# Optimization experiments

Measured on AMD Instinct MI355X. Metric: run time of the kernel, lower is better.

The kernel has to match this reference:

```python
import jax, jax.numpy as jnp
import numpy as np

L, HID, NH, NKV, HD, INTER = 16, 960, 15, 5, 64, 2560
VOCAB, NV, NT, PRE, SD = 49152, 192, 48, 241, 32
THETA, EPS, B = 100000.0, 1e-5, 16
GROUPS = NH // NKV


def setup_inputs() -> dict:
    key = jax.random.key(0)
    ks = jax.random.split(key, 20)
    s = 0.02
    rn = lambda k, shp: jax.random.normal(k, shp, jnp.float32) * s
    return {
        'vision_features': jax.random.normal(ks[0], (B, NV, HID), jnp.float32),
        'lang_token_ids': jax.random.randint(ks[1], (B, NT), 0, VOCAB),
        'lang_mask': jnp.ones((B, NT), dtype=bool),
        'state': jax.random.normal(ks[2], (B, SD), jnp.float32),
        'embed': rn(ks[3], (VOCAB, HID)),
        'state_w': rn(ks[4], (SD, HID)),
        'state_b': jnp.zeros((HID,), jnp.float32),
        'Wq': rn(ks[5], (L, HID, NH * HD)),
        'Wk': rn(ks[6], (L, HID, NKV * HD)),
        'Wv': rn(ks[7], (L, HID, NKV * HD)),
        'Wo': rn(ks[8], (L, NH * HD, HID)),
        'Wg': rn(ks[9], (L, HID, INTER)),
        'Wu': rn(ks[10], (L, HID, INTER)),
        'Wd': rn(ks[11], (L, INTER, HID)),
        'ln1': jnp.ones((L, HID), jnp.float32),
        'ln2': jnp.ones((L, HID), jnp.float32),
    }


def _rms(x, w):
    var = jnp.mean(jnp.square(x), axis=-1, keepdims=True)
    return x * jax.lax.rsqrt(var + EPS) * w


def _rotate_half(x):
    h = x.shape[-1] // 2
    return jnp.concatenate([-x[..., h:], x[..., :h]], axis=-1)


def _rope_tables(position_ids):
    # position_ids: [B, S] -> cos/sin: [B, S, HD]
    inv_freq = 1.0 / (THETA ** (jnp.arange(0, HD, 2, dtype=jnp.float32) / HD))
    freqs = position_ids.astype(jnp.float32)[..., None] * inv_freq  # [B,S,HD/2]
    emb = jnp.concatenate([freqs, freqs], axis=-1)
    return jnp.cos(emb), jnp.sin(emb)


def _apply_rope(x, cos, sin):
    # x: [B,S,H,D]; cos/sin: [B,S,D]
    return x * cos[:, :, None, :] + _rotate_half(x) * sin[:, :, None, :]


def _attention(q, k, v, mask2d):
    # q: [B,S,NH,HD]; k,v: [B,S,NKV,HD]; mask2d: [B,S,S] bool (query i, key j)
    kx = jnp.repeat(k, GROUPS, axis=2)  # GQA expand -> [B,S,NH,HD]
    vx = jnp.repeat(v, GROUPS, axis=2)
    scores = jnp.einsum('bihd,bjhd->bhij', q, kx) * (HD ** -0.5)
    big_neg = jnp.finfo(jnp.float32).min
    scores = jnp.where(mask2d[:, None, :, :], scores, big_neg)
    probs = jax.nn.softmax(scores, axis=-1)
    out = jnp.einsum('bhij,bjhd->bihd', probs, vx)
    return out.reshape(q.shape[0], q.shape[1], NH * HD)


def reference(vision_features, lang_token_ids, lang_mask, state,
              embed, state_w, state_b, Wq, Wk, Wv, Wo, Wg, Wu, Wd, ln1, ln2):
    lang_emb = embed[lang_token_ids] * jnp.sqrt(jnp.float32(HID))  # [B,NT,HID]
    state_emb = (state @ state_w + state_b)[:, None, :]            # [B,1,HID]
    x = jnp.concatenate([vision_features, lang_emb, state_emb], axis=1)  # [B,PRE,HID]

    pad = jnp.concatenate([jnp.ones((B, NV), bool), lang_mask.astype(bool),
                           jnp.ones((B, 1), bool)], axis=1)  # [B,PRE]
    position_ids = jnp.clip(jnp.cumsum(pad.astype(jnp.int32), axis=1) - 1, 0, None)
    cos, sin = _rope_tables(position_ids)

    att_marks = jnp.zeros((PRE,), jnp.int32).at[NV + NT:].set(1)
    cum = jnp.cumsum(att_marks)
    att2d = cum[None, :] >= cum[:, None]  # [S_q, S_kv]: key cum <= query cum
    pad2d = pad[:, :, None] & pad[:, None, :]
    mask2d = att2d[None, :, :] & pad2d  # [B,S,S]

    def layer(x, w):
        h = _rms(x, w['ln1'])
        S = h.shape[1]
        q = (h @ w['Wq']).reshape(B, S, NH, HD)
        k = (h @ w['Wk']).reshape(B, S, NKV, HD)
        v = (h @ w['Wv']).reshape(B, S, NKV, HD)
        q = _apply_rope(q, cos, sin)
        k = _apply_rope(k, cos, sin)
        a = _attention(q, k, v, mask2d)
        x = x + a @ w['Wo']
        h2 = _rms(x, w['ln2'])
        m = (jax.nn.silu(h2 @ w['Wg']) * (h2 @ w['Wu'])) @ w['Wd']
        return x + m, (k, v)

    weights = {'Wq': Wq, 'Wk': Wk, 'Wv': Wv, 'Wo': Wo,
               'Wg': Wg, 'Wu': Wu, 'Wd': Wd, 'ln1': ln1, 'ln2': ln2}
    _, (keys, values) = jax.lax.scan(layer, x, weights)
    # keys/values: [L, B, PRE, NKV, HD]
    return keys, values
```

## Files before the change

### kernel.cpp

```cpp
#include <hip/hip_runtime.h>
#include <hip/hip_bf16.h>

namespace {

typedef __bf16 bf16_t;
typedef __bf16 bf16x8 __attribute__((ext_vector_type(8)));
typedef __bf16 bf16x4 __attribute__((ext_vector_type(4)));
typedef float f32x4 __attribute__((ext_vector_type(4)));

constexpr int kL     = 16;
constexpr int kHid   = 960;
constexpr int kNH    = 15;
constexpr int kNKV   = 5;
constexpr int kHD    = 64;
constexpr int kInter = 2560;
constexpr int kNV    = 192;
constexpr int kNT    = 48;
constexpr int kPre   = 241;
constexpr int kSD    = 32;
constexpr int kB     = 16;
constexpr int kTok   = kB * kPre;
constexpr int kTokP  = 3968;
constexpr int kQKV   = 1600;
constexpr float kEps = 1e-5f;
constexpr float kSqrtHid = 30.98386677f;

constexpr size_t kWoOff     = (size_t)1664 * 960;
constexpr size_t kWgOff     = kWoOff + (size_t)1024 * 960;
constexpr size_t kWuOff     = kWgOff + (size_t)2560 * 960;
constexpr size_t kWdOff     = kWuOff + (size_t)2560 * 960;
constexpr size_t kWPerLayer = kWdOff + (size_t)1024 * 2560;

__device__ __forceinline__ void gload16(const bf16_t* g, bf16_t* l) {
  __builtin_amdgcn_global_load_lds((const __attribute__((address_space(1))) void*)g,
                                   (__attribute__((address_space(3))) void*)l, 16, 0, 0);
}

__device__ __forceinline__ void xcd_tile(int& bx, int& by) {
  int nbx = gridDim.x;
  int nwg = nbx * gridDim.y;
  int orig = blockIdx.y * nbx + blockIdx.x;
  int q = nwg >> 3, r = nwg & 7;
  int xcd = orig & 7, pos = orig >> 3;
  int swz = (xcd < r) ? (xcd * (q + 1) + pos) : (r * (q + 1) + (xcd - r) * q + pos);
  bx = swz % nbx;
  by = swz / nbx;
}

__global__ void build_x_kernel(const float* __restrict__ vision,
                               const int*   __restrict__ tokens,
                               const float* __restrict__ state,
                               const float* __restrict__ embed,
                               const float* __restrict__ sw,
                               const float* __restrict__ sb,
                               float* __restrict__ x, bf16_t* __restrict__ xb) {
  int idx = blockIdx.x * blockDim.x + threadIdx.x;
  if (idx >= kTok * kHid) return;
  int t = idx / kHid, c = idx - t * kHid;
  int b = t / kPre, s = t - b * kPre;
  float v;
  if (s < kNV) {
    v = vision[((size_t)b * kNV + s) * kHid + c];
  } else if (s < kNV + kNT) {
    int tok = tokens[b * kNT + (s - kNV)];
    v = embed[(size_t)tok * kHid + c] * kSqrtHid;
  } else {
    float acc = sb[c];
#pragma unroll
    for (int i = 0; i < kSD; ++i) acc += state[b * kSD + i] * sw[i * kHid + c];
    v = acc;
  }
  x[idx] = v;
  xb[idx] = (bf16_t)v;
}

__global__ __launch_bounds__(256)
void rowssq_kernel(const float* __restrict__ x, float* __restrict__ ssq) {
  int t = blockIdx.x;
  int tid = threadIdx.x;
  const float* xr = x + (size_t)t * kHid;
  float4 v = make_float4(0.f, 0.f, 0.f, 0.f);
  if (tid < 240) v = ((const float4*)xr)[tid];
  float ss = v.x * v.x + v.y * v.y + v.z * v.z + v.w * v.w;
#pragma unroll
  for (int off = 32; off; off >>= 1) ss += __shfl_xor(ss, off);
  __shared__ float part[4];
  if ((tid & 63) == 0) part[tid >> 6] = ss;
  __syncthreads();
  if (tid == 0) ssq[t] = part[0] + part[1] + part[2] + part[3];
}

__global__ void rope_table_kernel(float* __restrict__ cosT, float* __restrict__ sinT) {
  int idx = blockIdx.x * blockDim.x + threadIdx.x;
  if (idx >= kPre * 32) return;
  int s = idx >> 5, fi = idx & 31;
  float inv = __expf(-(2.0f * (float)fi / (float)kHD) * __logf(100000.0f));
  float fr = (float)s * inv;
  cosT[idx] = cosf(fr);
  sinT[idx] = sinf(fr);
}

__device__ void transpose_tile(const float* __restrict__ src, bf16_t* __restrict__ dst,
                               const float* __restrict__ lnw, int K, int N, int tile) {
  __shared__ float ts[64][65];
  int ntn = N >> 6;
  int tk = tile / ntn, tn = tile - tk * ntn;
  int t = threadIdx.x;
  int r = t >> 2, c0 = (t & 3) << 4;
  const float* sp = src + (size_t)((tk << 6) + r) * N + (tn << 6) + c0;
  float4 a = ((const float4*)sp)[0];
  float4 b = ((const float4*)sp)[1];
  float4 c = ((const float4*)sp)[2];
  float4 d = ((const float4*)sp)[3];
  ts[r][c0 + 0] = a.x;  ts[r][c0 + 1] = a.y;  ts[r][c0 + 2] = a.z;  ts[r][c0 + 3] = a.w;
  ts[r][c0 + 4] = b.x;  ts[r][c0 + 5] = b.y;  ts[r][c0 + 6] = b.z;  ts[r][c0 + 7] = b.w;
  ts[r][c0 + 8] = c.x;  ts[r][c0 + 9] = c.y;  ts[r][c0 +10] = c.z;  ts[r][c0 +11] = c.w;
  ts[r][c0 +12] = d.x;  ts[r][c0 +13] = d.y;  ts[r][c0 +14] = d.z;  ts[r][c0 +15] = d.w;
  __syncthreads();
  float wv[16];
#pragma unroll
  for (int i = 0; i < 16; ++i) wv[i] = lnw ? lnw[(tk << 6) + c0 + i] : 1.f;
  bf16_t* dp = dst + (size_t)((tn << 6) + r) * K + (tk << 6) + c0;
  bf16x8 o0, o1;
#pragma unroll
  for (int i = 0; i < 8; ++i) o0[i] = (bf16_t)(ts[c0 + i][r] * wv[i]);
#pragma unroll
  for (int i = 0; i < 8; ++i) o1[i] = (bf16_t)(ts[c0 + 8 + i][r] * wv[8 + i]);
  *(bf16x8*)dp = o0;
  *(bf16x8*)(dp + 8) = o1;
}

__global__ __launch_bounds__(256)
void wconv_kernel(const float* __restrict__ Wq, const float* __restrict__ Wk,
                  const float* __restrict__ Wv, const float* __restrict__ Wo,
                  const float* __restrict__ Wg, const float* __restrict__ Wu,
                  const float* __restrict__ Wd, const float* __restrict__ ln1,
                  const float* __restrict__ ln2, bf16_t* __restrict__ wall) {
  int bid = blockIdx.x;
  int l = bid / 2400, t = bid - l * 2400;
  bf16_t* wl = wall + (size_t)l * kWPerLayer;
  const float* w1 = ln1 + (size_t)l * kHid;
  const float* w2 = ln2 + (size_t)l * kHid;
  if      (t < 225)  transpose_tile(Wq + (size_t)l * 921600, wl, w1, 960, 960, t);
  else if (t < 300)  transpose_tile(Wk + (size_t)l * 307200, wl + (size_t)960 * 960, w1, 960, 320, t - 225);
  else if (t < 375)  transpose_tile(Wv + (size_t)l * 307200, wl + (size_t)1280 * 960, w1, 960, 320, t - 300);
  else if (t < 600)  transpose_tile(Wo + (size_t)l * 921600, wl + kWoOff, nullptr, 960, 960, t - 375);
  else if (t < 1200) transpose_tile(Wg + (size_t)l * 2457600, wl + kWgOff, w2, 960, 2560, t - 600);
  else if (t < 1800) transpose_tile(Wu + (size_t)l * 2457600, wl + kWuOff, w2, 960, 2560, t - 1200);
  else               transpose_tile(Wd + (size_t)l * 2457600, wl + kWdOff, nullptr, 2560, 960, t - 1800);
}


__global__ __launch_bounds__(256, 4)
void gemm_qkv_kernel(const bf16_t* __restrict__ A, const float* __restrict__ ssq,
                     const bf16_t* __restrict__ Bt,
                     bf16_t* __restrict__ qkv, float* __restrict__ outk,
                     float* __restrict__ outv,
                     const float* __restrict__ cosT, const float* __restrict__ sinT) {
  constexpr int K = kHid;
  constexpr int NT = K / 32;
  __shared__ alignas(16) bf16_t As[2][4096];
  __shared__ alignas(16) bf16_t Bs[2][2048];
  int tid = threadIdx.x;
  int bx, by;
  xcd_tile(bx, by);
  int m0 = by * 128, n0 = bx * 64;
  int lane = tid & 63, wid = tid >> 6;
  int wr = wid * 32;
  int r0 = tid >> 2, c0 = (tid & 3) * 8;
  int lr = lane & 15, lg = lane >> 4;

  const bf16_t* a0 = A + (size_t)(m0 + r0) * K + c0;
  const bf16_t* a1 = a0 + (size_t)64 * K;
  const bf16_t* b0 = Bt + (size_t)(n0 + r0) * K + c0;

  f32x4 acc[2][4];
#pragma unroll
  for (int m = 0; m < 2; ++m)
#pragma unroll
    for (int n = 0; n < 4; ++n) acc[m][n] = (f32x4){0.f, 0.f, 0.f, 0.f};

  int arow0 = (wr + lr) * 32 + lg * 8;
  int brow0 = lr * 32 + lg * 8;

  gload16(a0, &As[0][tid * 8]);
  gload16(a1, &As[0][2048 + tid * 8]);
  gload16(b0, &Bs[0][tid * 8]);
  __syncthreads();

  int cur = 0;
  for (int t = 0; t < NT; ++t) {
    if (t + 1 < NT) {
      int k1 = (t + 1) * 32;
      gload16(a0 + k1, &As[cur ^ 1][tid * 8]);
      gload16(a1 + k1, &As[cur ^ 1][2048 + tid * 8]);
      gload16(b0 + k1, &Bs[cur ^ 1][tid * 8]);
    }
    bf16x8 af[2], bfr[4];
#pragma unroll
    for (int m = 0; m < 2; ++m) af[m] = *(const bf16x8*)&As[cur][arow0 + m * 16 * 32];
#pragma unroll
    for (int n = 0; n < 4; ++n) bfr[n] = *(const bf16x8*)&Bs[cur][brow0 + n * 16 * 32];
#pragma unroll
    for (int m = 0; m < 2; ++m)
#pragma unroll
      for (int n = 0; n < 4; ++n)
        acc[m][n] = __builtin_amdgcn_mfma_f32_16x16x32_bf16(af[m], bfr[n], acc[m][n], 0, 0, 0);
    __syncthreads();
    cur ^= 1;
  }

  int cbase = n0;
  int cr4 = lg * 4;
  float srow[2][4];
#pragma unroll
  for (int m = 0; m < 2; ++m)
#pragma unroll
    for (int r = 0; r < 4; ++r)
      srow[m][r] = rsqrtf(ssq[m0 + wr + m * 16 + cr4 + r] * (1.f / 960.f) + kEps);

  if (cbase < 1280) {
    bool isQ = cbase < 960;
    float scale = isQ ? 0.125f : 1.0f;
#pragma unroll
    for (int m = 0; m < 2; ++m) {
      int row = m0 + wr + m * 16 + cr4;
#pragma unroll
      for (int r = 0; r < 4; ++r) {
        int rr = row + r;
        if (rr >= kTok) continue;
        int s = rr % kPre;
        bf16_t* qrow = qkv + (size_t)rr * kQKV + cbase;
        float* krow = outk + (size_t)rr * 320 + (cbase - 960);
#pragma unroll
        for (int n = 0; n < 2; ++n) {
          int d = n * 16 + lr;
          float c = cosT[s * 32 + d], sn = sinT[s * 32 + d];
          float lo = acc[m][n][r] * srow[m][r];
          float hi = acc[m][n + 2][r] * srow[m][r];
          float y0 = lo * c - hi * sn;
          float y1 = hi * c + lo * sn;
          qrow[d]      = (bf16_t)(y0 * scale);
          qrow[d + 32] = (bf16_t)(y1 * scale);
          if (!isQ) { krow[d] = y0; krow[d + 32] = y1; }
        }
      }
    }
  } else {
#pragma unroll
    for (int m = 0; m < 2; ++m) {
      int row = m0 + wr + m * 16 + cr4;
#pragma unroll
      for (int r = 0; r < 4; ++r) {
        int rr = row + r;
        if (rr >= kTok) continue;
        bf16_t* qrow = qkv + (size_t)rr * kQKV + cbase;
        float* vrow = outv + (size_t)rr * 320 + (cbase - 1280);
#pragma unroll
        for (int n = 0; n < 4; ++n) {
          int d = n * 16 + lr;
          float v = acc[m][n][r] * srow[m][r];
          qrow[d] = (bf16_t)v;
          vrow[d] = v;
        }
      }
    }
  }
}

__global__ __launch_bounds__(256, 4)
void gemm_res_kernel(const bf16_t* __restrict__ A, const bf16_t* __restrict__ Bt,
                     const float* __restrict__ src, float* __restrict__ C,
                     bf16_t* __restrict__ xb, float* __restrict__ ssq_out,
                     int M, int N, int K) {
  __shared__ alignas(16) bf16_t As[2][4096];
  __shared__ alignas(16) bf16_t Bs[2][2048];
  int tid = threadIdx.x;
  int bx, by;
  xcd_tile(bx, by);
  int m0 = by * 128, n0 = bx * 64;
  int lane = tid & 63, wid = tid >> 6;
  int wr = wid * 32;
  int r0 = tid >> 2, c0 = (tid & 3) * 8;
  int lr = lane & 15, lg = lane >> 4;

  const bf16_t* a0 = A + (size_t)(m0 + r0) * K + c0;
  const bf16_t* a1 = a0 + (size_t)64 * K;
  const bf16_t* b0 = Bt + (size_t)(n0 + r0) * K + c0;

  f32x4 acc[2][4];
#pragma unroll
  for (int m = 0; m < 2; ++m)
#pragma unroll
    for (int n = 0; n < 4; ++n) acc[m][n] = (f32x4){0.f, 0.f, 0.f, 0.f};

  int arow0 = (wr + lr) * 32 + lg * 8;
  int brow0 = lr * 32 + lg * 8;

  gload16(a0, &As[0][tid * 8]);
  gload16(a1, &As[0][2048 + tid * 8]);
  gload16(b0, &Bs[0][tid * 8]);
  __syncthreads();

  int NT = K / 32;
  int cur = 0;
  for (int t = 0; t < NT; ++t) {
    if (t + 1 < NT) {
      int k1 = (t + 1) * 32;
      gload16(a0 + k1, &As[cur ^ 1][tid * 8]);
      gload16(a1 + k1, &As[cur ^ 1][2048 + tid * 8]);
      gload16(b0 + k1, &Bs[cur ^ 1][tid * 8]);
    }
    bf16x8 af[2], bfr[4];
#pragma unroll
    for (int m = 0; m < 2; ++m) af[m] = *(const bf16x8*)&As[cur][arow0 + m * 16 * 32];
#pragma unroll
    for (int n = 0; n < 4; ++n) bfr[n] = *(const bf16x8*)&Bs[cur][brow0 + n * 16 * 32];
#pragma unroll
    for (int m = 0; m < 2; ++m)
#pragma unroll
      for (int n = 0; n < 4; ++n)
        acc[m][n] = __builtin_amdgcn_mfma_f32_16x16x32_bf16(af[m], bfr[n], acc[m][n], 0, 0, 0);
    __syncthreads();
    cur ^= 1;
  }

  int cr4 = lg * 4;
  float ps[2][4] = {};
#pragma unroll
  for (int m = 0; m < 2; ++m) {
    int row = m0 + wr + m * 16 + cr4;
#pragma unroll
    for (int n = 0; n < 4; ++n) {
      int col = n0 + n * 16 + lr;
#pragma unroll
      for (int r = 0; r < 4; ++r) {
        int rr = row + r;
        if (rr < M) {
          size_t off = (size_t)rr * N + col;
          float val = src[off] + acc[m][n][r];
          C[off] = val;
          xb[off] = (bf16_t)val;
          ps[m][r] += val * val;
        }
      }
    }
  }
#pragma unroll
  for (int m = 0; m < 2; ++m)
#pragma unroll
    for (int r = 0; r < 4; ++r) {
#pragma unroll
      for (int off = 8; off; off >>= 1) ps[m][r] += __shfl_xor(ps[m][r], off);
    }
  if (lr == 0) {
#pragma unroll
    for (int m = 0; m < 2; ++m) {
#pragma unroll
      for (int r = 0; r < 4; ++r) {
        int rr = m0 + wr + m * 16 + cr4 + r;
        if (rr < M) atomicAdd(&ssq_out[rr], ps[m][r]);
      }
    }
  }
}

__global__ __launch_bounds__(256)
void gemm_dual_kernel(const bf16_t* __restrict__ A, const float* __restrict__ ssq,
                      const bf16_t* __restrict__ Bg, const bf16_t* __restrict__ Bu,
                      bf16_t* __restrict__ act, int M, int K) {
  __shared__ alignas(16) bf16_t As[2][4096];
  __shared__ alignas(16) bf16_t Gs[2][2048];
  __shared__ alignas(16) bf16_t Us[2][2048];
  int tid = threadIdx.x;
  int bx, by;
  xcd_tile(bx, by);
  int m0 = by * 128, n0 = bx * 64;
  int lane = tid & 63, wid = tid >> 6;
  int wr = wid * 32;
  int r0 = tid >> 2, c0 = (tid & 3) * 8;
  int lr = lane & 15, lg = lane >> 4;

  const bf16_t* a0 = A + (size_t)(m0 + r0) * K + c0;
  const bf16_t* a1 = a0 + (size_t)64 * K;
  const bf16_t* g0 = Bg + (size_t)(n0 + r0) * K + c0;
  const bf16_t* u0 = Bu + (size_t)(n0 + r0) * K + c0;

  f32x4 accg[2][4], accu[2][4];
#pragma unroll
  for (int m = 0; m < 2; ++m)
#pragma unroll
    for (int n = 0; n < 4; ++n) {
      accg[m][n] = (f32x4){0.f, 0.f, 0.f, 0.f};
      accu[m][n] = (f32x4){0.f, 0.f, 0.f, 0.f};
    }

  int arow0 = (wr + lr) * 32 + lg * 8;
  int brow0 = lr * 32 + lg * 8;

  gload16(a0, &As[0][tid * 8]);
  gload16(a1, &As[0][2048 + tid * 8]);
  gload16(g0, &Gs[0][tid * 8]);
  gload16(u0, &Us[0][tid * 8]);
  __syncthreads();

  int NT = K / 32;
  int cur = 0;
  for (int t = 0; t < NT; ++t) {
    if (t + 1 < NT) {
      int k1 = (t + 1) * 32;
      gload16(a0 + k1, &As[cur ^ 1][tid * 8]);
      gload16(a1 + k1, &As[cur ^ 1][2048 + tid * 8]);
      gload16(g0 + k1, &Gs[cur ^ 1][tid * 8]);
      gload16(u0 + k1, &Us[cur ^ 1][tid * 8]);
    }
    bf16x8 af[2], bfr[4];
#pragma unroll
    for (int m = 0; m < 2; ++m) af[m] = *(const bf16x8*)&As[cur][arow0 + m * 16 * 32];
#pragma unroll
    for (int n = 0; n < 4; ++n) bfr[n] = *(const bf16x8*)&Gs[cur][brow0 + n * 16 * 32];
#pragma unroll
    for (int m = 0; m < 2; ++m)
#pragma unroll
      for (int n = 0; n < 4; ++n)
        accg[m][n] = __builtin_amdgcn_mfma_f32_16x16x32_bf16(af[m], bfr[n], accg[m][n], 0, 0, 0);
#pragma unroll
    for (int n = 0; n < 4; ++n) bfr[n] = *(const bf16x8*)&Us[cur][brow0 + n * 16 * 32];
#pragma unroll
    for (int m = 0; m < 2; ++m)
#pragma unroll
      for (int n = 0; n < 4; ++n)
        accu[m][n] = __builtin_amdgcn_mfma_f32_16x16x32_bf16(af[m], bfr[n], accu[m][n], 0, 0, 0);
    __syncthreads();
    cur ^= 1;
  }

  int cr4 = lg * 4;
  float srow[2][4];
#pragma unroll
  for (int m = 0; m < 2; ++m)
#pragma unroll
    for (int r = 0; r < 4; ++r)
      srow[m][r] = rsqrtf(ssq[m0 + wr + m * 16 + cr4 + r] * (1.f / 960.f) + kEps);
#pragma unroll
  for (int m = 0; m < 2; ++m) {
    int row = m0 + wr + m * 16 + cr4;
#pragma unroll
    for (int n = 0; n < 4; ++n) {
      int col = n0 + n * 16 + lr;
#pragma unroll
      for (int r = 0; r < 4; ++r) {
        int rr = row + r;
        if (rr < M) {
          float g = accg[m][n][r] * srow[m][r];
          float u = accu[m][n][r] * srow[m][r];
          float silu = g / (1.f + __expf(-g));
          act[(size_t)rr * kInter + col] = (bf16_t)(silu * u);
        }
      }
    }
  }
}

__global__ __launch_bounds__(256)
void attn_mfma_kernel(const bf16_t* __restrict__ qkv, bf16_t* __restrict__ aout) {
  int h = blockIdx.x, b = blockIdx.y;
  int kvh = h / 3;
  constexpr int LDK = 72;
  constexpr int LDV = 264;
  __shared__ alignas(16) bf16_t Ks[256 * LDK];
  __shared__ alignas(16) bf16_t Vt[64 * LDV];
  __shared__ alignas(16) bf16_t Ps[4][16 * LDV];
  const bf16_t* base = qkv + (size_t)b * kPre * kQKV;
  int tid = threadIdx.x;
  for (int i = tid; i < 2048; i += 256) {
    int j = i >> 3, c = (i & 7) * 8;
    bf16x8 k8, v8;
    if (j < kPre) {
      k8 = *(const bf16x8*)(base + (size_t)j * kQKV + 960 + kvh * 64 + c);
      v8 = *(const bf16x8*)(base + (size_t)j * kQKV + 1280 + kvh * 64 + c);
    } else {
#pragma unroll
      for (int e = 0; e < 8; ++e) { k8[e] = (bf16_t)0.f; v8[e] = (bf16_t)0.f; }
    }
    *(bf16x8*)&Ks[j * LDK + c] = k8;
#pragma unroll
    for (int e = 0; e < 8; ++e) Vt[(c + e) * LDV + j] = v8[e];
  }
  __syncthreads();
  int wid = tid >> 6, lane = tid & 63;
  int lr = lane & 15, lg = lane >> 4;
  bf16_t* myP = &Ps[wid][0];
  for (int qt = wid * 4; qt < wid * 4 + 4; ++qt) {
    int q0 = qt * 16;
    int qrow = q0 + lr; if (qrow > 240) qrow = 240;
    const bf16_t* qp = base + (size_t)qrow * kQKV + h * 64 + lg * 8;
    bf16x8 aq0 = *(const bf16x8*)qp;
    bf16x8 aq1 = *(const bf16x8*)(qp + 32);
    f32x4 sacc[16];
#pragma unroll
    for (int ct = 0; ct < 16; ++ct) sacc[ct] = (f32x4){0.f, 0.f, 0.f, 0.f};
#pragma unroll
    for (int ct = 0; ct < 16; ++ct) {
      int key = ct * 16 + lr;
      bf16x8 kb0 = *(const bf16x8*)&Ks[key * LDK + lg * 8];
      sacc[ct] = __builtin_amdgcn_mfma_f32_16x16x32_bf16(aq0, kb0, sacc[ct], 0, 0, 0);
      bf16x8 kb1 = *(const bf16x8*)&Ks[key * LDK + 32 + lg * 8];
      sacc[ct] = __builtin_amdgcn_mfma_f32_16x16x32_bf16(aq1, kb1, sacc[ct], 0, 0, 0);
    }
    float rmax[4] = {-1e30f, -1e30f, -1e30f, -1e30f};
#pragma unroll
    for (int ct = 0; ct < 16; ++ct) {
      int j = ct * 16 + lr;
#pragma unroll
      for (int r = 0; r < 4; ++r) {
        int q = q0 + lg * 4 + r;
        bool ok = (q < 240) ? (j < kPre) : (j == 240);
        float s = ok ? sacc[ct][r] : -1e30f;
        sacc[ct][r] = s;
        rmax[r] = fmaxf(rmax[r], s);
      }
    }
#pragma unroll
    for (int off = 8; off; off >>= 1) {
#pragma unroll
      for (int r = 0; r < 4; ++r) rmax[r] = fmaxf(rmax[r], __shfl_xor(rmax[r], off));
    }
    float rsum[4] = {0.f, 0.f, 0.f, 0.f};
#pragma unroll
    for (int ct = 0; ct < 16; ++ct) {
#pragma unroll
      for (int r = 0; r < 4; ++r) {
        float s = sacc[ct][r];
        float e = (s > -1e29f) ? __expf(s - rmax[r]) : 0.f;
        rsum[r] += e;
        myP[(lg * 4 + r) * LDV + ct * 16 + lr] = (bf16_t)e;
      }
    }
#pragma unroll
    for (int off = 8; off; off >>= 1) {
#pragma unroll
      for (int r = 0; r < 4; ++r) rsum[r] += __shfl_xor(rsum[r], off);
    }
    f32x4 oacc[4];
#pragma unroll
    for (int dt = 0; dt < 4; ++dt) oacc[dt] = (f32x4){0.f, 0.f, 0.f, 0.f};
#pragma unroll
    for (int ks = 0; ks < 8; ++ks) {
      bf16x8 pa = *(const bf16x8*)&myP[lr * LDV + ks * 32 + lg * 8];
#pragma unroll
      for (int dt = 0; dt < 4; ++dt) {
        bf16x8 vbf = *(const bf16x8*)&Vt[(dt * 16 + lr) * LDV + ks * 32 + lg * 8];
        oacc[dt] = __builtin_amdgcn_mfma_f32_16x16x32_bf16(pa, vbf, oacc[dt], 0, 0, 0);
      }
    }
    float linv[4];
#pragma unroll
    for (int r = 0; r < 4; ++r) linv[r] = 1.f / rsum[r];
#pragma unroll
    for (int dt = 0; dt < 4; ++dt) {
#pragma unroll
      for (int r = 0; r < 4; ++r) {
        int q = q0 + lg * 4 + r;
        if (q < kPre) {
          aout[((size_t)b * kPre + q) * kHid + h * 64 + dt * 16 + lr] =
              (bf16_t)(oacc[dt][r] * linv[r]);
        }
      }
    }
  }
}

}

extern "C" void kernel_launch(void* const* d_in, const int* in_sizes, int n_in,
                              void* d_out, int out_size, void* d_ws, size_t ws_size,
                              hipStream_t stream) {
  const float* vision = (const float*)d_in[0];
  const int*   tokens = (const int*)d_in[1];
  const float* state = (const float*)d_in[3];
  const float* embed = (const float*)d_in[4];
  const float* sw    = (const float*)d_in[5];
  const float* sb    = (const float*)d_in[6];
  const float* Wq    = (const float*)d_in[7];
  const float* Wk    = (const float*)d_in[8];
  const float* Wv    = (const float*)d_in[9];
  const float* Wo    = (const float*)d_in[10];
  const float* Wg    = (const float*)d_in[11];
  const float* Wu    = (const float*)d_in[12];
  const float* Wd    = (const float*)d_in[13];
  const float* ln1   = (const float*)d_in[14];
  const float* ln2   = (const float*)d_in[15];

  char* w = (char*)d_ws;
  float*  x      = (float*)w;   w += (size_t)kTokP * kHid * 4;
  bf16_t* xb     = (bf16_t*)w;  w += (size_t)kTokP * kHid * 2;
  bf16_t* qkv    = (bf16_t*)w;  w += (size_t)kTok * kQKV * 2;
  bf16_t* a_bf   = (bf16_t*)w;  w += (size_t)kTokP * kHid * 2;
  bf16_t* act_bf = (bf16_t*)w;  w += (size_t)kTokP * kInter * 2;
  bf16_t* wall   = (bf16_t*)w;  w += kWPerLayer * kL * 2;
  float*  cosT   = (float*)w;   w += (size_t)kPre * 32 * 4;
  float*  sinT   = (float*)w;   w += (size_t)kPre * 32 * 4;
  float*  ssqA   = (float*)w;   w += (size_t)(kL + 1) * kTokP * 4;
  float*  ssqB   = (float*)w;   w += (size_t)kL * kTokP * 4;

  float* out_k = (float*)d_out;
  float* out_v = out_k + (size_t)kL * kTok * 320;

  hipMemsetAsync(ssqA, 0, (size_t)(2 * kL + 1) * kTokP * 4, stream);

  build_x_kernel<<<(kTok * kHid + 255) / 256, 256, 0, stream>>>(
      vision, tokens, state, embed, sw, sb, x, xb);
  rowssq_kernel<<<kTok, 256, 0, stream>>>(x, ssqA);
  rope_table_kernel<<<(kPre * 32 + 255) / 256, 256, 0, stream>>>(cosT, sinT);
  wconv_kernel<<<2400 * kL, 256, 0, stream>>>(Wq, Wk, Wv, Wo, Wg, Wu, Wd, ln1, ln2, wall);

  for (int l = 0; l < kL; ++l) {
    bf16_t* wl = wall + (size_t)l * kWPerLayer;
    float* ssq1  = ssqA + (size_t)l * kTokP;
    float* ssq1n = ssqA + (size_t)(l + 1) * kTokP;
    float* ssq2  = ssqB + (size_t)l * kTokP;
    gemm_qkv_kernel<<<dim3(25, 31), 256, 0, stream>>>(
        xb, ssq1, wl, qkv, out_k + (size_t)l * kTok * 320,
        out_v + (size_t)l * kTok * 320, cosT, sinT);
    attn_mfma_kernel<<<dim3(15, 16), 256, 0, stream>>>(qkv, a_bf);
    gemm_res_kernel<<<dim3(15, 31), 256, 0, stream>>>(
        a_bf, wl + kWoOff, x, x, xb, ssq2, kTok, kHid, kHid);
    gemm_dual_kernel<<<dim3(40, 31), 256, 0, stream>>>(
        xb, ssq2, wl + kWgOff, wl + kWuOff, act_bf, kTok, kHid);
    gemm_res_kernel<<<dim3(15, 31), 256, 0, stream>>>(
        act_bf, wl + kWdOff, x, x, xb, ssq1n, kTok, kHid, kInter);
  }
}
```

Before: 3.494 ms.

## Deepen GEMM pipeline to 4-stage LDS ring with prefetch distance two

Replaces the double-buffered LDS staging in the QKV and residual GEMM kernels with a four-slot ring, prefetching two K-tiles ahead. Explicit vmcnt waits and a single barrier per iteration replace the two __syncthreads per iteration. The goal is to hide global-load latency better and cut synchronisation. In exchange LDS use doubles to 48KB per block and the min-blocks hint is dropped, which can lower occupancy. Correctness depends on gload16 being direct-to-LDS loads counted by vmcnt and on the exact count of outstanding loads.

```diff
diff --git a/kernel.cpp b/kernel.cpp
--- a/kernel.cpp
+++ b/kernel.cpp
@@ -151,7 +151,7 @@
 }
 
 
-__global__ __launch_bounds__(256, 4)
+__global__ __launch_bounds__(256)
 void gemm_qkv_kernel(const bf16_t* __restrict__ A, const float* __restrict__ ssq,
                      const bf16_t* __restrict__ Bt,
                      bf16_t* __restrict__ qkv, float* __restrict__ outk,
@@ -159,8 +159,8 @@
                      const float* __restrict__ cosT, const float* __restrict__ sinT) {
   constexpr int K = kHid;
   constexpr int NT = K / 32;
-  __shared__ alignas(16) bf16_t As[2][4096];
-  __shared__ alignas(16) bf16_t Bs[2][2048];
+  __shared__ alignas(16) bf16_t As[4][4096];
+  __shared__ alignas(16) bf16_t Bs[4][2048];
   int tid = threadIdx.x;
   int bx, by;
   xcd_tile(bx, by);
@@ -186,16 +186,25 @@
   gload16(a0, &As[0][tid * 8]);
   gload16(a1, &As[0][2048 + tid * 8]);
   gload16(b0, &Bs[0][tid * 8]);
-  __syncthreads();
-
-  int cur = 0;
+  gload16(a0 + 32, &As[1][tid * 8]);
+  gload16(a1 + 32, &As[1][2048 + tid * 8]);
+  gload16(b0 + 32, &Bs[1][tid * 8]);
+
   for (int t = 0; t < NT; ++t) {
-    if (t + 1 < NT) {
-      int k1 = (t + 1) * 32;
-      gload16(a0 + k1, &As[cur ^ 1][tid * 8]);
-      gload16(a1 + k1, &As[cur ^ 1][2048 + tid * 8]);
-      gload16(b0 + k1, &Bs[cur ^ 1][tid * 8]);
-    }
+    int cur = t & 3;
+    if (t + 2 < NT) {
+      int k2 = (t + 2) * 32;
+      int nb = (t + 2) & 3;
+      gload16(a0 + k2, &As[nb][tid * 8]);
+      gload16(a1 + k2, &As[nb][2048 + tid * 8]);
+      gload16(b0 + k2, &Bs[nb][tid * 8]);
+      asm volatile("s_waitcnt vmcnt(6)" ::: "memory");
+    } else if (t + 1 < NT) {
+      asm volatile("s_waitcnt vmcnt(3)" ::: "memory");
+    } else {
+      asm volatile("s_waitcnt vmcnt(0)" ::: "memory");
+    }
+    __builtin_amdgcn_s_barrier();
     bf16x8 af[2], bfr[4];
 #pragma unroll
     for (int m = 0; m < 2; ++m) af[m] = *(const bf16x8*)&As[cur][arow0 + m * 16 * 32];
@@ -206,8 +215,6 @@
 #pragma unroll
       for (int n = 0; n < 4; ++n)
         acc[m][n] = __builtin_amdgcn_mfma_f32_16x16x32_bf16(af[m], bfr[n], acc[m][n], 0, 0, 0);
-    __syncthreads();
-    cur ^= 1;
   }
 
   int cbase = n0;
@@ -268,13 +275,13 @@
   }
 }
 
-__global__ __launch_bounds__(256, 4)
+__global__ __launch_bounds__(256)
 void gemm_res_kernel(const bf16_t* __restrict__ A, const bf16_t* __restrict__ Bt,
                      const float* __restrict__ src, float* __restrict__ C,
                      bf16_t* __restrict__ xb, float* __restrict__ ssq_out,
                      int M, int N, int K) {
-  __shared__ alignas(16) bf16_t As[2][4096];
-  __shared__ alignas(16) bf16_t Bs[2][2048];
+  __shared__ alignas(16) bf16_t As[4][4096];
+  __shared__ alignas(16) bf16_t Bs[4][2048];
   int tid = threadIdx.x;
   int bx, by;
   xcd_tile(bx, by);
@@ -300,17 +307,26 @@
   gload16(a0, &As[0][tid * 8]);
   gload16(a1, &As[0][2048 + tid * 8]);
   gload16(b0, &Bs[0][tid * 8]);
-  __syncthreads();
+  gload16(a0 + 32, &As[1][tid * 8]);
+  gload16(a1 + 32, &As[1][2048 + tid * 8]);
+  gload16(b0 + 32, &Bs[1][tid * 8]);
 
   int NT = K / 32;
-  int cur = 0;
   for (int t = 0; t < NT; ++t) {
-    if (t + 1 < NT) {
-      int k1 = (t + 1) * 32;
-      gload16(a0 + k1, &As[cur ^ 1][tid * 8]);
-      gload16(a1 + k1, &As[cur ^ 1][2048 + tid * 8]);
-      gload16(b0 + k1, &Bs[cur ^ 1][tid * 8]);
-    }
+    int cur = t & 3;
+    if (t + 2 < NT) {
+      int k2 = (t + 2) * 32;
+      int nb = (t + 2) & 3;
+      gload16(a0 + k2, &As[nb][tid * 8]);
+      gload16(a1 + k2, &As[nb][2048 + tid * 8]);
+      gload16(b0 + k2, &Bs[nb][tid * 8]);
+      asm volatile("s_waitcnt vmcnt(6)" ::: "memory");
+    } else if (t + 1 < NT) {
+      asm volatile("s_waitcnt vmcnt(3)" ::: "memory");
+    } else {
+      asm volatile("s_waitcnt vmcnt(0)" ::: "memory");
+    }
+    __builtin_amdgcn_s_barrier();
     bf16x8 af[2], bfr[4];
 #pragma unroll
     for (int m = 0; m < 2; ++m) af[m] = *(const bf16x8*)&As[cur][arow0 + m * 16 * 32];
@@ -321,8 +337,6 @@
 #pragma unroll
       for (int n = 0; n < 4; ++n)
         acc[m][n] = __builtin_amdgcn_mfma_f32_16x16x32_bf16(af[m], bfr[n], acc[m][n], 0, 0, 0);
-    __syncthreads();
-    cur ^= 1;
   }
 
   int cr4 = lg * 4;
```

Measured after the change: 3.529 ms. No clear change (+1.0%).
